# Kernel tuning notes

Measured on AMD Instinct MI355X. Metric: run time of the kernel, lower is better.

The kernel has to match this reference:

```python
import jax, jax.numpy as jnp
import numpy as np

PI = float(np.pi)


def _lsa_cols(cost):
    """Jonker-Volgenant / Hungarian on a square cost matrix (numpy float64).
    Returns col_ind such that (arange(n), col_ind) is the optimal assignment,
    matching scipy.optimize.linear_sum_assignment for a square matrix."""
    n = cost.shape[0]
    C = np.zeros((n + 1, n + 1), dtype=np.float64)
    C[1:, 1:] = cost
    u = np.zeros(n + 1)
    v = np.zeros(n + 1)
    p = np.zeros(n + 1, dtype=np.int64)  # p[j] = row matched to column j (1-indexed)
    for i in range(1, n + 1):
        p[0] = i
        j0 = 0
        minv = np.full(n + 1, np.inf)
        way = np.zeros(n + 1, dtype=np.int64)
        used = np.zeros(n + 1, dtype=bool)
        while True:
            used[j0] = True
            i0 = p[j0]
            cur = C[i0] - u[i0] - v
            upd = (~used) & (cur < minv)
            minv = np.where(upd, cur, minv)
            way[upd] = j0
            masked = np.where(used, np.inf, minv)
            j1 = int(np.argmin(masked))
            delta = masked[j1]
            u[p[used]] += delta
            v[used] -= delta
            minv[~used] -= delta
            j0 = j1
            if p[j0] == 0:
                break
        while j0:
            j1 = way[j0]
            p[j0] = p[j1]
            j0 = j1
    col_to_row = p[1:] - 1  # row assigned to each column
    col_ind = np.empty(n, dtype=np.int64)
    col_ind[col_to_row] = np.arange(n)
    return col_ind


def _batched_assignment(input, target):
    # cdist p=2 : (B, N, N)
    diff = input[:, :, None, :] - target[:, None, :, :]
    cost = jnp.sqrt(jnp.sum(diff * diff, axis=-1))
    cost_np = np.asarray(cost, dtype=np.float64)
    # serial per-sample Hungarian solve (mirrors the original scipy loop)
    cols = np.stack([_lsa_cols(cost_np[b]) for b in range(cost_np.shape[0])], axis=0)
    return jnp.asarray(cols)  # (B, N)


def setup_inputs() -> dict:
    key = jax.random.key(0)
    k1, k2 = jax.random.split(key)
    B, N, D = 128, 128, 5
    return {
        "input": jax.random.normal(k1, (B, N, D), dtype=jnp.float32),
        "target": jax.random.normal(k2, (B, N, D), dtype=jnp.float32),
    }


def reference(input, target):
    cols = _batched_assignment(input, target)  # (B, N), constant w.r.t. grads
    # row_ind is identity (square matrix), so aligned_pred == input;
    # aligned_true = target gathered by the optimal columns.
    aligned_true = jnp.take_along_axis(target, cols[:, :, None], axis=1)
    d = input - aligned_true
    x_loss = jnp.mean(d[..., 0] ** 2)
    y_loss = jnp.mean(d[..., 1] ** 2)
    E_loss = jnp.mean(d[..., 2] ** 2)
    theta_loss = jnp.mean(d[..., 3] ** 2)
    phi_diff = jnp.remainder(d[..., 4] + PI, 2.0 * PI) - PI  # wrap to (-pi, pi]
    phi_loss = jnp.mean(phi_diff ** 2)
    total_loss = x_loss + y_loss + E_loss + theta_loss + phi_loss
    # [total, x, y, E, theta, phi]
    return jnp.stack([total_loss, x_loss, y_loss, E_loss, theta_loss, phi_loss])
```

## Files before the change

kernel.cpp:

```cpp
#include <hip/hip_runtime.h>

#define NN 128
#define NB 128
#define ND 5
#define INFV 3.4028235e38f

__device__ __forceinline__ float wrap_phi(float x) {
  const float PI_F   = 3.14159265358979323846f;
  const float TWO_PI = 6.28318530717958647692f;
  float t = x + PI_F;
  float w = t - floorf(t * (1.0f / TWO_PI)) * TWO_PI;
  return w - PI_F;
}

#define DPP_SRC_INF(x, ctrl, rmask)                                           \
  __int_as_float(__builtin_amdgcn_update_dpp(                                 \
      0x7f800000, __float_as_int(x), (ctrl), (rmask), 0xF, false))

#define DPP_MIN_STEP(x, ctrl, rmask) x = fminf(x, DPP_SRC_INF(x, ctrl, rmask))

#define DPP_MIN2_STEP(x1, x2, ctrl, rmask)                                    \
  { float _a1 = DPP_SRC_INF(x1, ctrl, rmask);                                 \
    float _a2 = DPP_SRC_INF(x2, ctrl, rmask);                                 \
    float _t  = fmaxf(x1, _a1);                                               \
    x1 = fminf(x1, _a1);                                                      \
    x2 = fminf(fminf(x2, _a2), _t); }

__device__ __forceinline__ int rl_i(int v, int lane) {
  return __builtin_amdgcn_readlane(v, lane);
}
__device__ __forceinline__ float rl_f(float v, int lane) {
  return __int_as_float(__builtin_amdgcn_readlane(__float_as_int(v), lane));
}

__device__ __forceinline__ float wave_min_bcast(float x) {
  DPP_MIN_STEP(x, 0xB1,  0xF);
  DPP_MIN_STEP(x, 0x4E,  0xF);
  DPP_MIN_STEP(x, 0x141, 0xF);
  DPP_MIN_STEP(x, 0x140, 0xF);
  DPP_MIN_STEP(x, 0x142, 0xA);
  DPP_MIN_STEP(x, 0x143, 0xC);
  return rl_f(x, 63);
}

__device__ __forceinline__ void wave_min2_bcast(float &x1, float &x2) {
  DPP_MIN2_STEP(x1, x2, 0xB1,  0xF);
  DPP_MIN2_STEP(x1, x2, 0x4E,  0xF);
  DPP_MIN2_STEP(x1, x2, 0x141, 0xF);
  DPP_MIN2_STEP(x1, x2, 0x140, 0xF);
  DPP_MIN2_STEP(x1, x2, 0x142, 0xA);
  DPP_MIN2_STEP(x1, x2, 0x143, 0xC);
  x1 = rl_f(x1, 63);
  x2 = rl_f(x2, 63);
}

__global__ __launch_bounds__(64) void set2set_hungarian(
    const float* __restrict__ inp, const float* __restrict__ tgt,
    float* __restrict__ sums)
{
  const int b = blockIdx.x;
  const int lane = threadIdx.x;

  __shared__ __align__(16) float Csh[NN * NN];
  __shared__ float inpS[NN * ND];
  __shared__ int   rowOwner[NN + 1];
  __shared__ float uFree[NN + 1];

  const float* inB = inp + (size_t)b * NN * ND;
  const float* tgB = tgt + (size_t)b * NN * ND;

  for (int idx = lane; idx < NN * ND; idx += 64) inpS[idx] = inB[idx];
  for (int idx = lane; idx <= NN; idx += 64) { rowOwner[idx] = 0x7fffffff; uFree[idx] = 0.f; }
  __syncthreads();

  const int jA = 2 * lane;
  const int jB = 2 * lane + 1;
  const int c1A = jA + 1, c1B = jB + 1;

  float tA[ND], tB[ND];
  #pragma unroll
  for (int d = 0; d < ND; ++d) { tA[d] = tgB[jA * ND + d]; tB[d] = tgB[jB * ND + d]; }

  float vA = INFV, vB = INFV;
  int   rmA = 1,  rmB = 1;
  #pragma unroll 4
  for (int i = 0; i < NN; ++i) {
    float sA = 0.f, sB = 0.f;
    #pragma unroll
    for (int d = 0; d < ND; ++d) {
      float x = inpS[i * ND + d];
      float da = x - tA[d]; sA = fmaf(da, da, sA);
      float db = x - tB[d]; sB = fmaf(db, db, sB);
    }
    float cA = sqrtf(sA), cB = sqrtf(sB);
    ((float2*)(Csh + i * NN))[lane] = make_float2(cA, cB);
    if (cA < vA) { vA = cA; rmA = i + 1; }
    if (cB < vB) { vB = cB; rmB = i + 1; }
  }
  __syncthreads();

  atomicMin(&rowOwner[rmA], c1A);
  atomicMin(&rowOwner[rmB], c1B);
  __syncthreads();

  int   pA = (rowOwner[rmA] == c1A) ? rmA : 0;
  int   pB = (rowOwner[rmB] == c1B) ? rmB : 0;
  float uA = 0.f, uB = 0.f;
  int   wayA = 0, wayB = 0;

  {
    unsigned long long mtA = __ballot(pA != 0);
    unsigned long long mtB = __ballot(pB != 0);
    while (mtA | mtB) {
      int l, slot;
      if (mtA) { l = __ffsll(mtA) - 1; mtA &= mtA - 1ull; slot = 0; }
      else     { l = __ffsll(mtB) - 1; mtB &= mtB - 1ull; slot = 1; }
      int owner = l;
      int i = rl_i(slot ? pB : pA, owner);
      const float2 c = ((const float2*)(Csh + (i - 1) * NN))[lane];
      float rA_ = c.x - vA, rB_ = c.y - vB;
      if (lane == owner) { if (slot) rB_ = INFV; else rA_ = INFV; }
      float mu = wave_min_bcast(fminf(rA_, rB_));
      bool selA = (lane == owner) && (slot == 0);
      bool selB = (lane == owner) && (slot == 1);
      vA -= selA ? mu : 0.f;   vB -= selB ? mu : 0.f;
      uA  = selA ? mu : uA;    uB  = selB ? mu : uB;
    }
  }

  unsigned long long remLo = __ballot(rowOwner[1 + lane]  == 0x7fffffff);
  unsigned long long remHi = __ballot(rowOwner[65 + lane] == 0x7fffffff);
  unsigned long long dijLo = 0ull, dijHi = 0ull;

  #pragma unroll 1
  for (int pass = 0; pass < 2; ++pass) {
    unsigned long long inLo = remLo, inHi = remHi;
    unsigned long long outLo = 0ull, outHi = 0ull;
    while (inLo | inHi) {
      int i;
      if (inLo) { int t = __ffsll(inLo) - 1; inLo &= inLo - 1ull; i = t + 1; }
      else      { int t = __ffsll(inHi) - 1; inHi &= inHi - 1ull; i = t + 65; }

      const float2 c = ((const float2*)(Csh + (i - 1) * NN))[lane];
      float rcA = c.x - vA, rcB = c.y - vB;
      float m1 = fminf(rcA, rcB), m2 = fmaxf(rcA, rcB);
      float candv = m1;
      int   candc = (rcA <= rcB) ? c1A : c1B;
      wave_min2_bcast(m1, m2);

      unsigned long long msk = __ballot(candv == m1);
      int l = __ffsll(msk) - 1;
      int j1 = rl_i(candc, l);
      int owner = l, slot = (j1 - 1) & 1;

      int   i0   = rl_i(slot ? pB : pA, owner);
      float uOld = rl_f(slot ? uB : uA, owner);

      float dv = m2 - m1;
      bool selA = (lane == owner) && (slot == 0);
      bool selB = (lane == owner) && (slot == 1);
      vA -= selA ? dv : 0.f;   vB -= selB ? dv : 0.f;
      pA  = selA ? i  : pA;    pB  = selB ? i  : pB;
      uA  = selA ? m2 : uA;    uB  = selB ? m2 : uB;

      if (i0 != 0) {
        if (lane == 0) uFree[i0] = uOld;
        if (i0 <= 64) outLo |= 1ull << (i0 - 1);
        else          outHi |= 1ull << (i0 - 65);
      }
    }
    remLo = outLo; remHi = outHi;
  }
  dijLo = remLo; dijHi = remHi;

  while (dijLo | dijHi) {
    int i;
    if (dijLo) { int t = __ffsll(dijLo) - 1; dijLo &= dijLo - 1ull; i = t + 1; }
    else       { int t = __ffsll(dijHi) - 1; dijHi &= dijHi - 1ull; i = t + 65; }
    float uf = uFree[i];

    float mA = INFV, mB = INFV;
    bool usedA = false, usedB = false;
    float ucur = uf;
    int   j0 = 0, i0 = i;
    float ui0 = uf;
    int   jfree = 0;

    for (int guard = 0; guard <= NN + 1; ++guard) {
      usedA |= (j0 == c1A);
      usedB |= (j0 == c1B);
      const float2 c = ((const float2*)(Csh + (i0 - 1) * NN))[lane];
      float curA = c.x - ui0 - vA;
      float curB = c.y - ui0 - vB;
      bool updA = !usedA && (curA < mA);
      bool updB = !usedB && (curB < mB);
      mA = updA ? curA : mA;  wayA = updA ? j0 : wayA;
      mB = updB ? curB : mB;  wayB = updB ? j0 : wayB;

      float mAx = usedA ? INFV : mA;
      float mBx = usedB ? INFV : mB;
      float candv = fminf(mAx, mBx);
      int   candc = (mAx <= mBx) ? c1A : c1B;
      float delta = wave_min_bcast(candv);
      unsigned long long msk = __ballot(candv == delta);
      int l = __ffsll(msk) - 1;
      int j1 = rl_i(candc, l);
      int owner = l, slot = (j1 - 1) & 1;

      ucur += delta;
      float dA = usedA ? delta : 0.f;
      float dB = usedB ? delta : 0.f;
      vA -= dA; uA += dA; mA -= (delta - dA);
      vB -= dB; uB += dB; mB -= (delta - dB);

      int pj1 = rl_i(slot ? pB : pA, owner);
      if (pj1 == 0) { jfree = j1; break; }
      ui0 = rl_f(slot ? uB : uA, owner);
      j0 = j1; i0 = pj1;
    }

    int jj = jfree;
    for (int g = 0; g < NN + 1 && jj != 0; ++g) {
      int owner = (jj - 1) >> 1, slot = (jj - 1) & 1;
      int wj = slot ? rl_i(wayB, owner) : rl_i(wayA, owner);
      int pnew; float unew;
      if (wj == 0) { pnew = i; unew = ucur; }
      else {
        int o2 = (wj - 1) >> 1, s2 = (wj - 1) & 1;
        pnew = s2 ? rl_i(pB, o2) : rl_i(pA, o2);
        unew = s2 ? rl_f(uB, o2) : rl_f(uA, o2);
      }
      bool selA = (lane == owner) && (slot == 0);
      bool selB = (lane == owner) && (slot == 1);
      pA = selA ? pnew : pA;  uA = selA ? unew : uA;
      pB = selB ? pnew : pB;  uB = selB ? unew : uB;
      jj = wj;
    }
  }

  int rA = pA - 1;
  int rB = pB - 1;
  float acc[ND];
  #pragma unroll
  for (int d = 0; d < ND; ++d) {
    float dA = inpS[rA * ND + d] - tA[d];
    float dB = inpS[rB * ND + d] - tB[d];
    if (d == 4) { dA = wrap_phi(dA); dB = wrap_phi(dB); }
    acc[d] = dA * dA + dB * dB;
  }
  #pragma unroll
  for (int d = 0; d < ND; ++d) {
    float s = acc[d];
    #pragma unroll
    for (int off = 32; off > 0; off >>= 1) s += __shfl_xor(s, off);
    if (lane == 0) atomicAdd(&sums[d], s);
  }
}

__global__ void set2set_finalize(const float* __restrict__ sums, float* __restrict__ out) {
  const float inv = 1.0f / (128.0f * 128.0f);
  float x  = sums[0] * inv;
  float y  = sums[1] * inv;
  float E  = sums[2] * inv;
  float th = sums[3] * inv;
  float ph = sums[4] * inv;
  out[1] = x; out[2] = y; out[3] = E; out[4] = th; out[5] = ph;
  out[0] = x + y + E + th + ph;
}

extern "C" void kernel_launch(void* const* d_in, const int* in_sizes, int n_in,
                              void* d_out, int out_size, void* d_ws, size_t ws_size,
                              hipStream_t stream) {
  const float* inp = (const float*)d_in[0];
  const float* tgt = (const float*)d_in[1];
  float* out  = (float*)d_out;
  float* sums = (float*)d_ws;

  hipMemsetAsync(sums, 0, ND * sizeof(float), stream);
  set2set_hungarian<<<dim3(NB), dim3(64), 0, stream>>>(inp, tgt, sums);
  set2set_finalize<<<dim3(1), dim3(1), 0, stream>>>(sums, out);
}
```

Baseline: 402.3 us.

## Use lazy dual updates in Dijkstra augmentation and fuse readlane selects

Switches the shortest augmenting path loop from updating the duals u/v and minv eagerly on every step to the lazy form: distances stay absolute and dual adjustments for used columns are applied once after the path is found. It also picks the candidate's p and u values per lane before the wave reduction, so the owner's values come from a direct readlane instead of a slot-dependent select followed by readlane. Both cut per-iteration VALU work and dependency depth in a serial, latency-bound loop. Changing the update order can shift floating-point rounding in the duals.

```diff
diff --git a/kernel.cpp b/kernel.cpp
--- a/kernel.cpp
+++ b/kernel.cpp
@@ -130,7 +130,6 @@
 
   unsigned long long remLo = __ballot(rowOwner[1 + lane]  == 0x7fffffff);
   unsigned long long remHi = __ballot(rowOwner[65 + lane] == 0x7fffffff);
-  unsigned long long dijLo = 0ull, dijHi = 0ull;
 
   #pragma unroll 1
   for (int pass = 0; pass < 2; ++pass) {
@@ -145,16 +144,18 @@
       float rcA = c.x - vA, rcB = c.y - vB;
       float m1 = fminf(rcA, rcB), m2 = fmaxf(rcA, rcB);
       float candv = m1;
-      int   candc = (rcA <= rcB) ? c1A : c1B;
+      bool  aMin  = (rcA <= rcB);
+      int   candc = aMin ? c1A : c1B;
+      int   candp = aMin ? pA : pB;
+      float candu = aMin ? uA : uB;
       wave_min2_bcast(m1, m2);
 
       unsigned long long msk = __ballot(candv == m1);
       int l = __ffsll(msk) - 1;
-      int j1 = rl_i(candc, l);
+      int   j1   = rl_i(candc, l);
+      int   i0   = rl_i(candp, l);
+      float uOld = rl_f(candu, l);
       int owner = l, slot = (j1 - 1) & 1;
-
-      int   i0   = rl_i(slot ? pB : pA, owner);
-      float uOld = rl_f(slot ? uB : uA, owner);
 
       float dv = m2 - m1;
       bool selA = (lane == owner) && (slot == 0);
@@ -171,7 +172,7 @@
     }
     remLo = outLo; remHi = outHi;
   }
-  dijLo = remLo; dijHi = remHi;
+  unsigned long long dijLo = remLo, dijHi = remHi;
 
   while (dijLo | dijHi) {
     int i;
@@ -179,45 +180,51 @@
     else       { int t = __ffsll(dijHi) - 1; dijHi &= dijHi - 1ull; i = t + 65; }
     float uf = uFree[i];
 
-    float mA = INFV, mB = INFV;
+    float dA_ = INFV, dB_ = INFV;
     bool usedA = false, usedB = false;
-    float ucur = uf;
     int   j0 = 0, i0 = i;
-    float ui0 = uf;
+    float tshift = 0.f - uf;
+    float minVal = 0.f;
     int   jfree = 0;
 
     for (int guard = 0; guard <= NN + 1; ++guard) {
-      usedA |= (j0 == c1A);
-      usedB |= (j0 == c1B);
       const float2 c = ((const float2*)(Csh + (i0 - 1) * NN))[lane];
-      float curA = c.x - ui0 - vA;
-      float curB = c.y - ui0 - vB;
-      bool updA = !usedA && (curA < mA);
-      bool updB = !usedB && (curB < mB);
-      mA = updA ? curA : mA;  wayA = updA ? j0 : wayA;
-      mB = updB ? curB : mB;  wayB = updB ? j0 : wayB;
-
-      float mAx = usedA ? INFV : mA;
-      float mBx = usedB ? INFV : mB;
+      float curA = tshift + c.x - vA;
+      float curB = tshift + c.y - vB;
+      bool updA = !usedA && (curA < dA_);
+      bool updB = !usedB && (curB < dB_);
+      dA_ = updA ? curA : dA_;  wayA = updA ? j0 : wayA;
+      dB_ = updB ? curB : dB_;  wayB = updB ? j0 : wayB;
+
+      float mAx = usedA ? INFV : dA_;
+      float mBx = usedB ? INFV : dB_;
       float candv = fminf(mAx, mBx);
-      int   candc = (mAx <= mBx) ? c1A : c1B;
-      float delta = wave_min_bcast(candv);
-      unsigned long long msk = __ballot(candv == delta);
+      bool  aMin  = (mAx <= mBx);
+      int   candc = aMin ? c1A : c1B;
+      int   candp = aMin ? pA : pB;
+      float candu = aMin ? uA : uB;
+
+      minVal = wave_min_bcast(candv);
+      unsigned long long msk = __ballot(candv == minVal);
       int l = __ffsll(msk) - 1;
-      int j1 = rl_i(candc, l);
-      int owner = l, slot = (j1 - 1) & 1;
-
-      ucur += delta;
-      float dA = usedA ? delta : 0.f;
-      float dB = usedB ? delta : 0.f;
-      vA -= dA; uA += dA; mA -= (delta - dA);
-      vB -= dB; uB += dB; mB -= (delta - dB);
-
-      int pj1 = rl_i(slot ? pB : pA, owner);
+      int j1  = rl_i(candc, l);
+      int pj1 = rl_i(candp, l);
+      float uj = rl_f(candu, l);
       if (pj1 == 0) { jfree = j1; break; }
-      ui0 = rl_f(slot ? uB : uA, owner);
+
+      usedA |= (j1 == c1A);
+      usedB |= (j1 == c1B);
+      tshift = minVal - uj;
       j0 = j1; i0 = pj1;
     }
+
+    {
+      float adjA = dA_ - minVal;
+      float adjB = dB_ - minVal;
+      vA += usedA ? adjA : 0.f;   uA -= usedA ? adjA : 0.f;
+      vB += usedB ? adjB : 0.f;   uB -= usedB ? adjB : 0.f;
+    }
+    float ucur = uf + minVal;
 
     int jj = jfree;
     for (int g = 0; g < NN + 1 && jj != 0; ++g) {
```

New measurement: 414.7 us. 1.03x slower.
